# Kernel optimization log

Hardware: AMD Instinct MI355X
Metric: run time of the kernel (lower is better)

The kernel has to match this reference:

```python
import jax, jax.numpy as jnp
import numpy as np

DIM = 1024
AUX = 3
B, S = 32, 1024
ENC_D = DIM * AUX  # 3072


def setup_inputs() -> dict:
    key = jax.random.key(0)
    ks = jax.random.split(key, 5)
    sc1 = 1.0 / np.sqrt(DIM * (AUX + 1))
    sc3 = 1.0 / np.sqrt(ENC_D)
    return {
        "hidden_state": jax.random.normal(ks[0], (B, DIM), jnp.float32),
        "encoder_outputs": jax.random.normal(ks[1], (B, S, ENC_D), jnp.float32),
        "W1": jax.random.normal(ks[2], (DIM, DIM * (AUX + 1)), jnp.float32) * sc1,
        "b1": jnp.zeros((DIM,), jnp.float32),
        "w2": jax.random.normal(ks[3], (1, DIM), jnp.float32) * (1.0 / np.sqrt(DIM)),
        "W3": jax.random.normal(ks[4], (DIM, ENC_D), jnp.float32) * sc3,
        "b3": jnp.zeros((DIM,), jnp.float32),
    }


def reference(hidden_state, encoder_outputs, W1, b1, w2, W3, b3):
    # hidden_state: (B, dim); encoder_outputs: (B, S, dim*aux)
    Bsz, Slen, _ = encoder_outputs.shape
    h = jnp.broadcast_to(hidden_state[:, None, :], (Bsz, Slen, hidden_state.shape[-1]))
    inputs = jnp.concatenate([encoder_outputs, h], axis=2)  # (B, S, dim*(aux+1))
    # score MLP: tanh(linear1) -> linear2 (no bias)
    hidden = jnp.tanh(jnp.einsum('bsf,df->bsd', inputs, W1) + b1)  # (B, S, dim)
    e = jnp.einsum('bsd,od->bso', hidden, w2)[..., 0]  # (B, S)
    alpha = jax.nn.softmax(e, axis=1)
    context = jnp.einsum('bs,bsf->bf', alpha, encoder_outputs)  # (B, dim*aux)
    return jnp.einsum('bf,df->bd', context, W3) + b3  # (B, dim)
```

## Files before the change

kernel.cpp:

```cpp
#include <hip/hip_runtime.h>
#include <hip/hip_bf16.h>


typedef float          fx4 __attribute__((ext_vector_type(4)));
typedef short          sv8 __attribute__((ext_vector_type(8)));
typedef unsigned short uv4 __attribute__((ext_vector_type(4)));
typedef unsigned int   ui4 __attribute__((ext_vector_type(4)));

__device__ __forceinline__ unsigned short f2bf(float x) {
  unsigned u = __float_as_uint(x);
  return (unsigned short)((u + 0x7FFFu + ((u >> 16) & 1u)) >> 16);
}

__device__ __forceinline__ unsigned cvtpk(float lo, float hi) {
  unsigned r;
  asm("v_cvt_pk_bf16_f32 %0, %1, %2" : "=v"(r) : "v"(lo), "v"(hi));
  return r;
}
__device__ __forceinline__ ui4 pack8(fx4 a, fx4 b) {
  ui4 v;
  v[0] = cvtpk(a[0], a[1]); v[1] = cvtpk(a[2], a[3]);
  v[2] = cvtpk(b[0], b[1]); v[3] = cvtpk(b[2], b[3]);
  return v;
}

__global__ void convw1_kernel(const float* __restrict__ W1, unsigned short* __restrict__ W1a) {
  int id = blockIdx.x * 256 + threadIdx.x;
  int d = id / 768, fi = id - d * 768;
  fx4 v = ((const fx4*)W1)[d * 1024 + fi];
  uv4 r; r[0] = f2bf(v[0]); r[1] = f2bf(v[1]); r[2] = f2bf(v[2]); r[3] = f2bf(v[3]);
  ((uv4*)W1a)[d * 768 + fi] = r;
}

__global__ void hbias_kernel(const float* __restrict__ hs, const float* __restrict__ W1,
                             const float* __restrict__ b1, float* __restrict__ hb) {
  int idx = (blockIdx.x << 2) + (threadIdx.x >> 6);
  int lane = threadIdx.x & 63;
  int b = idx >> 10, d = idx & 1023;
  const fx4* hv = (const fx4*)hs;
  const fx4* wv = (const fx4*)W1;
  float s = 0.f;
#pragma unroll
  for (int i = 0; i < 4; ++i) {
    int k4 = lane + (i << 6);
    fx4 h = hv[(b << 8) + k4];
    fx4 w = wv[d * 1024 + 768 + k4];
    s += h[0] * w[0] + h[1] * w[1] + h[2] * w[2] + h[3] * w[3];
  }
#pragma unroll
  for (int off = 32; off; off >>= 1) s += __shfl_xor(s, off);
  if (lane == 0) hb[idx] = s + b1[d];
}

__global__ __launch_bounds__(512, 2)
void gemm_score(const float* __restrict__ enc,
                const unsigned short* __restrict__ W1a,
                const float* __restrict__ hb,
                const float* __restrict__ w2,
                float* __restrict__ pe) {
  __shared__ __align__(16) unsigned short As[2][10240];
  __shared__ __align__(16) unsigned short Bs[2][8192];

  const int t = threadIdx.x;
  const int lane = t & 63, wid = t >> 6;
  const int wm = wid >> 2, wn = wid & 3;

  const int bid = blockIdx.x;
  const int lg = ((bid & 7) << 6) | (bid >> 3);
  const int mt = lg >> 2, ntile = lg & 3;
  const int row0 = mt << 8;
  const int col0 = ntile << 8;

  const fx4* encv = (const fx4*)enc;

  const int ar = t >> 1, ah = t & 1;
  const int agb = (row0 + ar) * 768 + ah * 4;
  const int awb = ar * 40 + ah * 16;

  const int l3 = lane >> 3, l7 = lane & 7;
  const int pre = l7 ^ l3;
  const unsigned short* bsrc0 =
      W1a + (size_t)(col0 + wid * 32 + 2 * l3 + (pre >> 2)) * 3072 + (pre & 3) * 8;
  const unsigned short* bsrc1 = bsrc0 + (size_t)16 * 3072;
  const int bdst0 = (wid * 16) * 64;
  const int bdst1 = (wid * 16 + 8) * 64;

  const int r15 = lane & 15, qv = lane >> 4;
  const int aro = (wm * 128 + r15) * 40 + qv * 8;
  const int cb = wn * 64 + r15;
  const int bro = (cb >> 1) * 64 + (((((cb & 1) << 2) + qv) ^ ((cb >> 1) & 7)) << 3);

  fx4 acc[8][4] = {};
  fx4 pa[2][4];

#define A_LOAD(s, kt) { _Pragma("unroll") for (int j = 0; j < 4; ++j) pa[s][j] = encv[agb + (kt) * 8 + j]; }
#define A_WRITE(s, buf) { *(ui4*)&As[buf][awb] = pack8(pa[s][0], pa[s][1]); \
                          *(ui4*)&As[buf][awb + 8] = pack8(pa[s][2], pa[s][3]); }
#define B_ISSUE(buf, kt)                                              \
  { __builtin_amdgcn_global_load_lds(                                 \
        (const __attribute__((address_space(1))) void*)(bsrc0 + (kt) * 32), \
        (__attribute__((address_space(3))) void*)&Bs[buf][bdst0], 16, 0, 0); \
    __builtin_amdgcn_global_load_lds(                                 \
        (const __attribute__((address_space(1))) void*)(bsrc1 + (kt) * 32), \
        (__attribute__((address_space(3))) void*)&Bs[buf][bdst1], 16, 0, 0); }
#define COMPUTE(p)                                                    \
  { sv8 af[8], bfv[4];                                                \
    _Pragma("unroll")                                                 \
    for (int mi = 0; mi < 8; ++mi) af[mi] = *(const sv8*)&As[p][aro + mi * 640]; \
    _Pragma("unroll")                                                 \
    for (int ni = 0; ni < 4; ++ni) bfv[ni] = *(const sv8*)&Bs[p][bro + ni * 512]; \
    _Pragma("unroll")                                                 \
    for (int mi = 0; mi < 8; ++mi)                                    \
      _Pragma("unroll")                                               \
      for (int ni = 0; ni < 4; ++ni)                                  \
        acc[mi][ni] = __builtin_amdgcn_mfma_f32_16x16x32_bf16(af[mi], bfv[ni], acc[mi][ni], 0, 0, 0); }
#define ITER(kt, p)                                                   \
  { COMPUTE(p)                                                        \
    if ((kt) < 95) { A_WRITE(p ^ 1, p ^ 1) }    \
    if ((kt) < 93) { A_LOAD(p ^ 1, (kt) + 3) }   \
    __builtin_amdgcn_s_barrier();                \
    if ((kt) < 94) {                                                  \
      B_ISSUE(p, (kt) + 2)                                            \
      asm volatile("s_waitcnt vmcnt(6)" ::: "memory");                \
    } else if ((kt) == 94) {                                          \
      asm volatile("s_waitcnt vmcnt(0)" ::: "memory");                \
    }                                                                 \
    asm volatile("s_waitcnt lgkmcnt(0)" ::: "memory");                \
    __builtin_amdgcn_s_barrier(); }

  A_LOAD(0, 0)
  A_LOAD(1, 1)
  B_ISSUE(0, 0)
  A_WRITE(0, 0)
  B_ISSUE(1, 1)
  A_LOAD(0, 2)
  asm volatile("s_waitcnt vmcnt(6)" ::: "memory");
  asm volatile("s_waitcnt lgkmcnt(0)" ::: "memory");
  __builtin_amdgcn_s_barrier();

  for (int kt2 = 0; kt2 < 48; ++kt2) {
    const int kt = kt2 * 2;
    ITER(kt, 0)
    ITER(kt + 1, 1)
  }

  const int b = row0 >> 10;
  float w2v[4], hbv[4];
#pragma unroll
  for (int ni = 0; ni < 4; ++ni) {
    int c = col0 + wn * 64 + ni * 16 + r15;
    w2v[ni] = w2[c];
    hbv[ni] = hb[(b << 10) + c];
  }
#pragma unroll
  for (int mi = 0; mi < 8; ++mi) {
#pragma unroll
    for (int j = 0; j < 4; ++j) {
      float pz = 0.f;
#pragma unroll
      for (int ni = 0; ni < 4; ++ni)
        pz += tanhf(acc[mi][ni][j] + hbv[ni]) * w2v[ni];
      pz += __shfl_xor(pz, 1); pz += __shfl_xor(pz, 2);
      pz += __shfl_xor(pz, 4); pz += __shfl_xor(pz, 8);
      if (r15 == 0) {
        int row = row0 + wm * 128 + mi * 16 + (qv << 2) + j;
        pe[(row << 4) + (ntile << 2) + wn] = pz;
      }
    }
  }
#undef A_LOAD
#undef A_WRITE
#undef B_ISSUE
#undef COMPUTE
#undef ITER
}

__global__ void softmax_kernel(const float* __restrict__ pe, float* __restrict__ alpha) {
  int b = blockIdx.x, t = threadIdx.x;
  int lane = t & 63, wid = t >> 6;
  float ev[4];
#pragma unroll
  for (int r = 0; r < 4; ++r) {
    int s = t + r * 256;
    const float* p = pe + ((b << 10) + s) * 16;
    float sum = 0.f;
#pragma unroll
    for (int i = 0; i < 16; ++i) sum += p[i];
    ev[r] = sum;
  }
  float m = fmaxf(fmaxf(ev[0], ev[1]), fmaxf(ev[2], ev[3]));
#pragma unroll
  for (int off = 32; off; off >>= 1) m = fmaxf(m, __shfl_xor(m, off));
  __shared__ float red[8];
  if (lane == 0) red[wid] = m;
  __syncthreads();
  m = fmaxf(fmaxf(red[0], red[1]), fmaxf(red[2], red[3]));
  float p4[4], ls = 0.f;
#pragma unroll
  for (int r = 0; r < 4; ++r) { p4[r] = expf(ev[r] - m); ls += p4[r]; }
#pragma unroll
  for (int off = 32; off; off >>= 1) ls += __shfl_xor(ls, off);
  if (lane == 0) red[4 + wid] = ls;
  __syncthreads();
  float inv = 1.0f / (red[4] + red[5] + red[6] + red[7]);
#pragma unroll
  for (int r = 0; r < 4; ++r) alpha[(b << 10) + t + r * 256] = p4[r] * inv;
}

__global__ void ctxpart_kernel(const float* __restrict__ enc, const float* __restrict__ alpha,
                               float* __restrict__ part) {
  int bid = blockIdx.x, b = bid >> 4, sc = bid & 15;
  int t = threadIdx.x;
  __shared__ float sal[64];
  if (t < 64) sal[t] = alpha[(b << 10) + (sc << 6) + t];
  __syncthreads();
  const fx4* ev = (const fx4*)enc;
  fx4 a0 = {}, a1 = {}, a2 = {};
  int base = ((b << 10) + (sc << 6)) * 768;
  for (int si = 0; si < 64; ++si) {
    float a = sal[si];
    const fx4* rp = ev + base + si * 768;
    a0 += a * rp[t];
    a1 += a * rp[256 + t];
    a2 += a * rp[512 + t];
  }
  fx4* pp = (fx4*)part;
  int pb = ((b << 4) + sc) * 768;
  pp[pb + t] = a0; pp[pb + 256 + t] = a1; pp[pb + 512 + t] = a2;
}

__global__ void ctxreduce_kernel(const float* __restrict__ part, float* __restrict__ ctx) {
  int j = blockIdx.x * 256 + threadIdx.x;
  int b = j / 768, fi = j - b * 768;
  const fx4* pp = (const fx4*)part;
  fx4 s = {};
#pragma unroll
  for (int i = 0; i < 16; ++i) s += pp[((b << 4) + i) * 768 + fi];
  ((fx4*)ctx)[b * 768 + fi] = s;
}

__global__ void final_kernel(const float* __restrict__ ctx, const float* __restrict__ W3,
                             const float* __restrict__ b3, float* __restrict__ out) {
  int idx = (blockIdx.x << 2) + (threadIdx.x >> 6);
  int lane = threadIdx.x & 63;
  int b = idx >> 10, d = idx & 1023;
  const fx4* cv = (const fx4*)ctx;
  const fx4* wv = (const fx4*)W3;
  float s = 0.f;
#pragma unroll
  for (int i = 0; i < 12; ++i) {
    int f4 = lane + (i << 6);
    fx4 c = cv[b * 768 + f4];
    fx4 w = wv[d * 768 + f4];
    s += c[0] * w[0] + c[1] * w[1] + c[2] * w[2] + c[3] * w[3];
  }
#pragma unroll
  for (int off = 32; off; off >>= 1) s += __shfl_xor(s, off);
  if (lane == 0) out[idx] = s + b3[d];
}

extern "C" void kernel_launch(void* const* d_in, const int* in_sizes, int n_in,
                              void* d_out, int out_size, void* d_ws, size_t ws_size,
                              hipStream_t stream) {
  const float* hs  = (const float*)d_in[0];
  const float* enc = (const float*)d_in[1];
  const float* W1  = (const float*)d_in[2];
  const float* b1  = (const float*)d_in[3];
  const float* w2  = (const float*)d_in[4];
  const float* W3  = (const float*)d_in[5];
  const float* b3  = (const float*)d_in[6];
  float* out = (float*)d_out;

  char* ws = (char*)d_ws;
  unsigned short* W1a = (unsigned short*)(ws);
  float* pe    = (float*)(ws + 6291456);
  float* alpha = (float*)(ws + 8388608);
  float* hb    = (float*)(ws + 8519680);
  float* ctx   = (float*)(ws + 8650752);
  float* part  = (float*)(ws + 9043968);

  convw1_kernel<<<3072, 256, 0, stream>>>(W1, W1a);
  hbias_kernel<<<8192, 256, 0, stream>>>(hs, W1, b1, hb);
  gemm_score<<<512, 512, 0, stream>>>(enc, W1a, hb, w2, pe);
  softmax_kernel<<<32, 256, 0, stream>>>(pe, alpha);
  ctxpart_kernel<<<512, 256, 0, stream>>>(enc, alpha, part);
  ctxreduce_kernel<<<96, 256, 0, stream>>>(part, ctx);
  final_kernel<<<8192, 256, 0, stream>>>(ctx, W3, b3, out);
}
```

Baseline: 415.7 us.

## Pre-convert encoder outputs to bf16 and stream both GEMM operands via LDS DMA

Adds a pass that converts encoder_outputs to bf16 in workspace. A new GEMM kernel then loads both A and B tiles with global_load_lds, using a triple-buffered A, a double-buffered B, split MFMA phases and s_setprio. The context reduction now reads the bf16 copy instead of fp32. This removes the in-register fp32 to bf16 conversion from the GEMM hot loop and halves the later encoder reads. In exchange it adds an extra full pass over encoder_outputs, needs a workspace of about 216 MB (otherwise the old path runs), and lowers the precision of the context sum.

```diff
diff --git a/kernel.cpp b/kernel.cpp
--- a/kernel.cpp
+++ b/kernel.cpp
@@ -11,7 +11,6 @@
   unsigned u = __float_as_uint(x);
   return (unsigned short)((u + 0x7FFFu + ((u >> 16) & 1u)) >> 16);
 }
-
 __device__ __forceinline__ unsigned cvtpk(float lo, float hi) {
   unsigned r;
   asm("v_cvt_pk_bf16_f32 %0, %1, %2" : "=v"(r) : "v"(lo), "v"(hi));
@@ -23,6 +22,11 @@
   v[2] = cvtpk(b[0], b[1]); v[3] = cvtpk(b[2], b[3]);
   return v;
 }
+
+#define GLD(srcp, dstp)                                               \
+  __builtin_amdgcn_global_load_lds(                                   \
+      (const __attribute__((address_space(1))) void*)(srcp),          \
+      (__attribute__((address_space(3))) void*)(dstp), 16, 0, 0)
 
 __global__ void convw1_kernel(const float* __restrict__ W1, unsigned short* __restrict__ W1a) {
   int id = blockIdx.x * 256 + threadIdx.x;
@@ -30,6 +34,13 @@
   fx4 v = ((const fx4*)W1)[d * 1024 + fi];
   uv4 r; r[0] = f2bf(v[0]); r[1] = f2bf(v[1]); r[2] = f2bf(v[2]); r[3] = f2bf(v[3]);
   ((uv4*)W1a)[d * 768 + fi] = r;
+}
+
+__global__ void convenc_kernel(const float* __restrict__ enc, unsigned short* __restrict__ ebf) {
+  int id = blockIdx.x * 256 + threadIdx.x;
+  fx4 a = ((const fx4*)enc)[2 * id];
+  fx4 b = ((const fx4*)enc)[2 * id + 1];
+  ((ui4*)ebf)[id] = pack8(a, b);
 }
 
 __global__ void hbias_kernel(const float* __restrict__ hs, const float* __restrict__ W1,
@@ -53,30 +64,141 @@
 }
 
 __global__ __launch_bounds__(512, 2)
-void gemm_score(const float* __restrict__ enc,
-                const unsigned short* __restrict__ W1a,
-                const float* __restrict__ hb,
-                const float* __restrict__ w2,
-                float* __restrict__ pe) {
+void gemm8(const unsigned short* __restrict__ Ag,
+           const unsigned short* __restrict__ Bg,
+           const float* __restrict__ hb,
+           const float* __restrict__ w2,
+           float* __restrict__ pe) {
+  __shared__ __align__(16) unsigned short Ab[3][16384];
+  __shared__ __align__(16) unsigned short Bb[2][16384];
+
+  const int t = threadIdx.x, lane = t & 63, wid = t >> 6;
+  const int wm = wid >> 2, wn = wid & 3;
+
+  const int bid = blockIdx.x;
+  const int lg = ((bid & 7) << 6) | (bid >> 3);
+  const int mt = lg >> 2, nt = lg & 3;
+  const int row0 = mt << 8, col0 = nt << 8;
+
+  const int l3 = lane >> 3, l7 = lane & 7;
+  const unsigned short* asrc = Ag + (size_t)(row0 + wid * 32 + l3) * 3072 + ((l7 ^ l3) << 3);
+  const unsigned short* bsrc = Bg + (size_t)(col0 + wid * 32 + l3) * 3072 + ((l7 ^ l3) << 3);
+  const int dstb = wid << 11;
+
+  const int r15 = lane & 15, qv = lane >> 4;
+  const int aB = (wm * 128 + r15) << 6;
+  const int bB = (wn * 64 + r15) << 6;
+  const int s0 = (qv ^ (r15 & 7)) << 3;
+  const int s1 = ((qv + 4) ^ (r15 & 7)) << 3;
+
+  fx4 acc[8][4] = {};
+  sv8 bfv[4];
+
+#define ST_B(BN, kt, g) GLD(bsrc + (g) * 24576 + (kt) * 64, &Bb[BN][dstb + ((g) << 9)])
+#define ST_A(AN, kt, g) GLD(asrc + (g) * 24576 + (kt) * 64, &Ab[AN][dstb + ((g) << 9)])
+
+#define PHASE(AB, BBUF, MH, KH, ISSUE)                                \
+  { sv8 af[4];                                                        \
+    const int sx = (KH) ? s1 : s0;                                    \
+    _Pragma("unroll")                                                 \
+    for (int mi = 0; mi < 4; ++mi)                                    \
+      af[mi] = *(const sv8*)&Ab[AB][aB + (((MH) * 64 + mi * 16) << 6) + sx]; \
+    if ((MH) == 0) {                                                  \
+      _Pragma("unroll")                                               \
+      for (int ni = 0; ni < 4; ++ni)                                  \
+        bfv[ni] = *(const sv8*)&Bb[BBUF][bB + ((ni * 16) << 6) + sx]; \
+    }                                                                 \
+    ISSUE                                                             \
+    __builtin_amdgcn_s_barrier();                                     \
+    asm volatile("s_waitcnt lgkmcnt(0)" ::: "memory");                \
+    __builtin_amdgcn_s_setprio(1);                                    \
+    _Pragma("unroll")                                                 \
+    for (int mi = 0; mi < 4; ++mi)                                    \
+      _Pragma("unroll")                                               \
+      for (int ni = 0; ni < 4; ++ni)                                  \
+        acc[(MH) * 4 + mi][ni] = __builtin_amdgcn_mfma_f32_16x16x32_bf16( \
+            af[mi], bfv[ni], acc[(MH) * 4 + mi][ni], 0, 0, 0);        \
+    __builtin_amdgcn_s_setprio(0);                                    \
+  }
+
+#define TILE(kt, AB, BBUF, BN, AN)                                    \
+  PHASE(AB, BBUF, 0, 0, { if ((kt) < 47) { ST_B(BN, (kt) + 1, 0); ST_B(BN, (kt) + 1, 1); } }) \
+  __builtin_amdgcn_s_barrier();                                       \
+  PHASE(AB, BBUF, 1, 0, { if ((kt) < 47) { ST_B(BN, (kt) + 1, 2); ST_B(BN, (kt) + 1, 3); } }) \
+  __builtin_amdgcn_s_barrier();                                       \
+  PHASE(AB, BBUF, 0, 1, { if ((kt) < 46) { ST_A(AN, (kt) + 2, 0); ST_A(AN, (kt) + 2, 1); } }) \
+  __builtin_amdgcn_s_barrier();                                       \
+  PHASE(AB, BBUF, 1, 1, { if ((kt) < 46) { ST_A(AN, (kt) + 2, 2); ST_A(AN, (kt) + 2, 3); } }) \
+  if ((kt) < 46)       { asm volatile("s_waitcnt vmcnt(4)" ::: "memory"); } \
+  else if ((kt) == 46) { asm volatile("s_waitcnt vmcnt(0)" ::: "memory"); } \
+  __builtin_amdgcn_s_barrier();
+
+  ST_B(0, 0, 0); ST_B(0, 0, 1); ST_B(0, 0, 2); ST_B(0, 0, 3);
+  ST_A(0, 0, 0); ST_A(0, 0, 1); ST_A(0, 0, 2); ST_A(0, 0, 3);
+  ST_A(1, 1, 0); ST_A(1, 1, 1); ST_A(1, 1, 2); ST_A(1, 1, 3);
+  asm volatile("s_waitcnt vmcnt(4)" ::: "memory");
+  __builtin_amdgcn_s_barrier();
+
+  for (int it = 0; it < 8; ++it) {
+    const int k6 = it * 6;
+    TILE(k6 + 0, 0, 0, 1, 2)
+    TILE(k6 + 1, 1, 1, 0, 0)
+    TILE(k6 + 2, 2, 0, 1, 1)
+    TILE(k6 + 3, 0, 1, 0, 2)
+    TILE(k6 + 4, 1, 0, 1, 0)
+    TILE(k6 + 5, 2, 1, 0, 1)
+  }
+
+  const int b = row0 >> 10;
+  float w2v[4], hbv[4];
+#pragma unroll
+  for (int ni = 0; ni < 4; ++ni) {
+    int c = col0 + wn * 64 + ni * 16 + r15;
+    w2v[ni] = w2[c];
+    hbv[ni] = hb[(b << 10) + c];
+  }
+#pragma unroll
+  for (int mi = 0; mi < 8; ++mi) {
+#pragma unroll
+    for (int j = 0; j < 4; ++j) {
+      float pz = 0.f;
+#pragma unroll
+      for (int ni = 0; ni < 4; ++ni)
+        pz += tanhf(acc[mi][ni][j] + hbv[ni]) * w2v[ni];
+      pz += __shfl_xor(pz, 1); pz += __shfl_xor(pz, 2);
+      pz += __shfl_xor(pz, 4); pz += __shfl_xor(pz, 8);
+      if (r15 == 0) {
+        int row = row0 + wm * 128 + mi * 16 + (qv << 2) + j;
+        pe[(row << 4) + (nt << 2) + wn] = pz;
+      }
+    }
+  }
+#undef ST_A
+#undef ST_B
+#undef PHASE
+#undef TILE
+}
+
+__global__ __launch_bounds__(512, 2)
+void gemm2(const float* __restrict__ enc,
+           const unsigned short* __restrict__ W1a,
+           const float* __restrict__ hb,
+           const float* __restrict__ w2,
+           float* __restrict__ pe) {
   __shared__ __align__(16) unsigned short As[2][10240];
   __shared__ __align__(16) unsigned short Bs[2][8192];
-
   const int t = threadIdx.x;
   const int lane = t & 63, wid = t >> 6;
   const int wm = wid >> 2, wn = wid & 3;
-
   const int bid = blockIdx.x;
   const int lg = ((bid & 7) << 6) | (bid >> 3);
   const int mt = lg >> 2, ntile = lg & 3;
   const int row0 = mt << 8;
   const int col0 = ntile << 8;
-
   const fx4* encv = (const fx4*)enc;
-
   const int ar = t >> 1, ah = t & 1;
   const int agb = (row0 + ar) * 768 + ah * 4;
   const int awb = ar * 40 + ah * 16;
-
   const int l3 = lane >> 3, l7 = lane & 7;
   const int pre = l7 ^ l3;
   const unsigned short* bsrc0 =
@@ -84,25 +206,17 @@
   const unsigned short* bsrc1 = bsrc0 + (size_t)16 * 3072;
   const int bdst0 = (wid * 16) * 64;
   const int bdst1 = (wid * 16 + 8) * 64;
-
   const int r15 = lane & 15, qv = lane >> 4;
   const int aro = (wm * 128 + r15) * 40 + qv * 8;
   const int cb = wn * 64 + r15;
   const int bro = (cb >> 1) * 64 + (((((cb & 1) << 2) + qv) ^ ((cb >> 1) & 7)) << 3);
-
   fx4 acc[8][4] = {};
   fx4 pa[2][4];
-
 #define A_LOAD(s, kt) { _Pragma("unroll") for (int j = 0; j < 4; ++j) pa[s][j] = encv[agb + (kt) * 8 + j]; }
 #define A_WRITE(s, buf) { *(ui4*)&As[buf][awb] = pack8(pa[s][0], pa[s][1]); \
                           *(ui4*)&As[buf][awb + 8] = pack8(pa[s][2], pa[s][3]); }
-#define B_ISSUE(buf, kt)                                              \
-  { __builtin_amdgcn_global_load_lds(                                 \
-        (const __attribute__((address_space(1))) void*)(bsrc0 + (kt) * 32), \
-        (__attribute__((address_space(3))) void*)&Bs[buf][bdst0], 16, 0, 0); \
-    __builtin_amdgcn_global_load_lds(                                 \
-        (const __attribute__((address_space(1))) void*)(bsrc1 + (kt) * 32), \
-        (__attribute__((address_space(3))) void*)&Bs[buf][bdst1], 16, 0, 0); }
+#define B_ISSUE(buf, kt) { GLD(bsrc0 + (kt) * 32, &Bs[buf][bdst0]); \
+                           GLD(bsrc1 + (kt) * 32, &Bs[buf][bdst1]); }
 #define COMPUTE(p)                                                    \
   { sv8 af[8], bfv[4];                                                \
     _Pragma("unroll")                                                 \
@@ -116,9 +230,9 @@
         acc[mi][ni] = __builtin_amdgcn_mfma_f32_16x16x32_bf16(af[mi], bfv[ni], acc[mi][ni], 0, 0, 0); }
 #define ITER(kt, p)                                                   \
   { COMPUTE(p)                                                        \
-    if ((kt) < 95) { A_WRITE(p ^ 1, p ^ 1) }    \
-    if ((kt) < 93) { A_LOAD(p ^ 1, (kt) + 3) }   \
-    __builtin_amdgcn_s_barrier();                \
+    if ((kt) < 95) { A_WRITE(p ^ 1, p ^ 1) }                          \
+    if ((kt) < 93) { A_LOAD(p ^ 1, (kt) + 3) }                        \
+    __builtin_amdgcn_s_barrier();                                     \
     if ((kt) < 94) {                                                  \
       B_ISSUE(p, (kt) + 2)                                            \
       asm volatile("s_waitcnt vmcnt(6)" ::: "memory");                \
@@ -127,7 +241,6 @@
     }                                                                 \
     asm volatile("s_waitcnt lgkmcnt(0)" ::: "memory");                \
     __builtin_amdgcn_s_barrier(); }
-
   A_LOAD(0, 0)
   A_LOAD(1, 1)
   B_ISSUE(0, 0)
@@ -137,13 +250,11 @@
   asm volatile("s_waitcnt vmcnt(6)" ::: "memory");
   asm volatile("s_waitcnt lgkmcnt(0)" ::: "memory");
   __builtin_amdgcn_s_barrier();
-
   for (int kt2 = 0; kt2 < 48; ++kt2) {
     const int kt = kt2 * 2;
     ITER(kt, 0)
     ITER(kt + 1, 1)
   }
-
   const int b = row0 >> 10;
   float w2v[4], hbv[4];
 #pragma unroll
@@ -205,6 +316,34 @@
   float inv = 1.0f / (red[4] + red[5] + red[6] + red[7]);
 #pragma unroll
   for (int r = 0; r < 4; ++r) alpha[(b << 10) + t + r * 256] = p4[r] * inv;
+}
+
+__global__ void ctxpart_bf_kernel(const unsigned short* __restrict__ ebf,
+                                  const float* __restrict__ alpha,
+                                  float* __restrict__ part) {
+  int bid = blockIdx.x, b = bid >> 4, sc = bid & 15;
+  int t = threadIdx.x;
+  __shared__ float sal[64];
+  if (t < 64) sal[t] = alpha[(b << 10) + (sc << 6) + t];
+  __syncthreads();
+  const ui4* ev = (const ui4*)ebf;
+  float a8[8] = {};
+  int base = ((b << 10) + (sc << 6)) * 384;
+  for (int si = 0; si < 64; ++si) {
+    float a = sal[si];
+    ui4 v = ev[base + si * 384 + t];
+#pragma unroll
+    for (int j = 0; j < 4; ++j) {
+      unsigned u = v[j];
+      a8[2 * j]     += a * __uint_as_float(u << 16);
+      a8[2 * j + 1] += a * __uint_as_float(u & 0xFFFF0000u);
+    }
+  }
+  fx4* pp = (fx4*)part;
+  int pb = ((b << 4) + sc) * 768 + t * 2;
+  fx4 o0 = {a8[0], a8[1], a8[2], a8[3]};
+  fx4 o1 = {a8[4], a8[5], a8[6], a8[7]};
+  pp[pb] = o0; pp[pb + 1] = o1;
 }
 
 __global__ void ctxpart_kernel(const float* __restrict__ enc, const float* __restrict__ alpha,
@@ -270,20 +409,41 @@
   const float* W3  = (const float*)d_in[5];
   const float* b3  = (const float*)d_in[6];
   float* out = (float*)d_out;
-
   char* ws = (char*)d_ws;
-  unsigned short* W1a = (unsigned short*)(ws);
-  float* pe    = (float*)(ws + 6291456);
-  float* alpha = (float*)(ws + 8388608);
-  float* hb    = (float*)(ws + 8519680);
-  float* ctx   = (float*)(ws + 8650752);
-  float* part  = (float*)(ws + 9043968);
-
-  convw1_kernel<<<3072, 256, 0, stream>>>(W1, W1a);
-  hbias_kernel<<<8192, 256, 0, stream>>>(hs, W1, b1, hb);
-  gemm_score<<<512, 512, 0, stream>>>(enc, W1a, hb, w2, pe);
-  softmax_kernel<<<32, 256, 0, stream>>>(pe, alpha);
-  ctxpart_kernel<<<512, 256, 0, stream>>>(enc, alpha, part);
-  ctxreduce_kernel<<<96, 256, 0, stream>>>(part, ctx);
-  final_kernel<<<8192, 256, 0, stream>>>(ctx, W3, b3, out);
-}
+
+  const size_t NEED_A = 216662016ULL;
+
+  if (ws_size >= NEED_A) {
+    unsigned short* ebf = (unsigned short*)(ws);
+    unsigned short* W1a = (unsigned short*)(ws + 201326592);
+    float* pe    = (float*)(ws + 207618048);
+    float* alpha = (float*)(ws + 209715200);
+    float* hb    = (float*)(ws + 209846272);
+    float* ctx   = (float*)(ws + 209977344);
+    float* part  = (float*)(ws + 210370560);
+
+    convw1_kernel<<<3072, 256, 0, stream>>>(W1, W1a);
+    convenc_kernel<<<49152, 256, 0, stream>>>(enc, ebf);
+    hbias_kernel<<<8192, 256, 0, stream>>>(hs, W1, b1, hb);
+    gemm8<<<512, 512, 0, stream>>>(ebf, W1a, hb, w2, pe);
+    softmax_kernel<<<32, 256, 0, stream>>>(pe, alpha);
+    ctxpart_bf_kernel<<<512, 384, 0, stream>>>(ebf, alpha, part);
+    ctxreduce_kernel<<<96, 256, 0, stream>>>(part, ctx);
+    final_kernel<<<8192, 256, 0, stream>>>(ctx, W3, b3, out);
+  } else {
+    unsigned short* W1a = (unsigned short*)(ws);
+    float* pe    = (float*)(ws + 6291456);
+    float* alpha = (float*)(ws + 8388608);
+    float* hb    = (float*)(ws + 8519680);
+    float* ctx   = (float*)(ws + 8650752);
+    float* part  = (float*)(ws + 9043968);
+
+    convw1_kernel<<<3072, 256, 0, stream>>>(W1, W1a);
+    hbias_kernel<<<8192, 256, 0, stream>>>(hs, W1, b1, hb);
+    gemm2<<<512, 512, 0, stream>>>(enc, W1a, hb, w2, pe);
+    softmax_kernel<<<32, 256, 0, stream>>>(pe, alpha);
+    ctxpart_kernel<<<512, 256, 0, stream>>>(enc, alpha, part);
+    ctxreduce_kernel<<<96, 256, 0, stream>>>(part, ctx);
+    final_kernel<<<8192, 256, 0, stream>>>(ctx, W3, b3, out);
+  }
+}
```

Measured after the change: 445.8 us. 7.2% more time.
